# Optimization experiments

Hardware: AMD Instinct MI355X
Metric: run time of the kernel (lower is better)

The kernel has to match this reference:

```python
import jax, jax.numpy as jnp
import numpy as np

G = 4
EPS = 1e-5

def group_norm(x, gamma, beta):
    B, C, D, H, W = x.shape
    xg = x.reshape(B, G, C // G, D, H, W)
    mu = xg.mean(axis=(2, 3, 4, 5), keepdims=True)
    var = xg.var(axis=(2, 3, 4, 5), keepdims=True)
    xn = ((xg - mu) * jax.lax.rsqrt(var + EPS)).reshape(B, C, D, H, W)
    return xn * gamma[None, :, None, None, None] + beta[None, :, None, None, None]

def conv3d(x, w, b):
    y = jax.lax.conv_general_dilated(x, w, (1, 1, 1), [(1, 1), (1, 1), (1, 1)],
                                     dimension_numbers=('NCDHW', 'OIDHW', 'NCDHW'))
    return y + b[None, :, None, None, None]

def deform_conv_hw(x, offset, w, b):
    # x: [B,C,D,H,W]; offset: [B, 2*27, D,H,W] -> per-tap (dh, dw); depth taps are rigid.
    B, C, D, H, W = x.shape
    off = offset.reshape(B, 27, 2, D, H, W)
    xp = jnp.pad(x, ((0, 0), (0, 0), (1, 1), (0, 0), (0, 0)))  # zero-pad depth only
    hh = jnp.arange(H, dtype=x.dtype)[None, None, :, None]
    ww = jnp.arange(W, dtype=x.dtype)[None, None, None, :]
    bi = jnp.arange(B)[:, None, None, None]
    di = jnp.arange(D)[None, :, None, None]
    out = jnp.zeros((B, w.shape[0], D, H, W), x.dtype)
    tap = 0
    for i in range(3):
        x_d = xp[:, :, i:i + D]  # depth-shifted view [B,C,D,H,W]
        for j in range(3):
            for k in range(3):
                hp = hh + (j - 1) + off[:, tap, 0]  # [B,D,H,W] fractional h position
                wp = ww + (k - 1) + off[:, tap, 1]
                h0 = jnp.floor(hp); w0 = jnp.floor(wp)
                h0i = h0.astype(jnp.int32); w0i = w0.astype(jnp.int32)
                lh = hp - h0; lw = wp - w0
                def gather(hi, wi):
                    m = ((hi >= 0) & (hi < H) & (wi >= 0) & (wi < W)).astype(x.dtype)
                    g = x_d[bi, :, di, jnp.clip(hi, 0, H - 1), jnp.clip(wi, 0, W - 1)]  # [B,D,H,W,C]
                    return g, m
                g00, m00 = gather(h0i, w0i)
                g01, m01 = gather(h0i, w0i + 1)
                g10, m10 = gather(h0i + 1, w0i)
                g11, m11 = gather(h0i + 1, w0i + 1)
                val = (((1 - lh) * (1 - lw) * m00)[..., None] * g00
                       + ((1 - lh) * lw * m01)[..., None] * g01
                       + (lh * (1 - lw) * m10)[..., None] * g10
                       + (lh * lw * m11)[..., None] * g11)
                out = out + jnp.einsum('bdhwc,oc->bodhw', val, w[:, :, i, j, k])
                tap += 1
    return out + b[None, :, None, None, None]

def setup_inputs():
    key = jax.random.key(0)
    ks = jax.random.split(key, 8)
    B, C, D, H, W = 1, 32, 24, 96, 96
    x = jax.random.normal(ks[0], (B, C, D, H, W), jnp.float32)
    g1 = jnp.ones((C,), jnp.float32); be1 = jnp.zeros((C,), jnp.float32)
    g2 = jnp.ones((C,), jnp.float32); be2 = jnp.zeros((C,), jnp.float32)
    ow1 = jax.random.normal(ks[1], (54, C, 3, 3, 3), jnp.float32) * 0.02
    ob1 = jnp.zeros((54,), jnp.float32)
    dw1 = jax.random.normal(ks[2], (C, C, 3, 3, 3), jnp.float32) * 0.05
    db1 = jnp.zeros((C,), jnp.float32)
    ow2 = jax.random.normal(ks[3], (54, C, 3, 3, 3), jnp.float32) * 0.02
    ob2 = jnp.zeros((54,), jnp.float32)
    dw2 = jax.random.normal(ks[4], (C, C, 3, 3, 3), jnp.float32) * 0.05
    db2 = jnp.zeros((C,), jnp.float32)
    return {"x": x, "g1": g1, "be1": be1, "g2": g2, "be2": be2,
            "ow1": ow1, "ob1": ob1, "dw1": dw1, "db1": db1,
            "ow2": ow2, "ob2": ob2, "dw2": dw2, "db2": db2}

def reference(x, g1, be1, g2, be2, ow1, ob1, dw1, db1, ow2, ob2, dw2, db2):
    h = jax.nn.relu(group_norm(x, g1, be1))
    h = deform_conv_hw(h, conv3d(h, ow1, ob1), dw1, db1)
    h = jax.nn.relu(group_norm(h, g2, be2))
    h = deform_conv_hw(h, conv3d(h, ow2, ob2), dw2, db2)
    return h + x
```

## Files before the change

### kernel.cpp

```cpp
#include <hip/hip_runtime.h>
#include <hip/hip_fp16.h>

#define CC   32
#define DD   24
#define HH   96
#define WW   96
#define HWC  (HH*WW)
#define DHW  (DD*HH*WW)
#define NG   4
#define CPG  (CC/NG)
#define OC1  54
#define GN_EPS 1e-5f
#define NBLK2 (DHW/128)
#define CHUNK2 (NBLK2/8)

typedef float  f32x4 __attribute__((ext_vector_type(4)));
typedef _Float16 f16x8 __attribute__((ext_vector_type(8)));
typedef unsigned int u32x4 __attribute__((ext_vector_type(4)));

union F16Frag { f16x8 v; __half2 h2[4]; };

__device__ __forceinline__ int swz_block(int bid) {
    return (bid % 8) * CHUNK2 + (bid / 8);
}

__global__ void pack_w(const float* __restrict__ src, _Float16* __restrict__ dst,
                       int O, int NT, int n) {
    int idx = blockIdx.x * 256 + threadIdx.x;
    if (idx >= n) return;
    int e    = idx & 7;
    int lane = (idx >> 3) & 63;
    int nt   = (idx >> 9) % NT;
    int tap  = (idx >> 9) / NT;
    int o = nt * 16 + (lane & 15);
    int c = (lane >> 4) * 8 + e;
    float v = (o < O) ? src[(o * CC + c) * 27 + tap] : 0.f;
    dst[idx] = (_Float16)v;
}

__global__ void gn_stats(const float* __restrict__ x, float* __restrict__ stats) {
    const int g = blockIdx.x >> 5;
    const int s = blockIdx.x & 31;
    const float4* base = (const float4*)(x + (size_t)g * CPG * DHW);
    const int n4 = CPG * DHW / 4;
    float s1 = 0.f, s2 = 0.f;
    for (int idx = s * 256 + threadIdx.x; idx < n4; idx += 32 * 256) {
        float4 v = base[idx];
        s1 += v.x + v.y + v.z + v.w;
        s2 += v.x * v.x + v.y * v.y + v.z * v.z + v.w * v.w;
    }
    for (int off = 32; off > 0; off >>= 1) {
        s1 += __shfl_down(s1, off);
        s2 += __shfl_down(s2, off);
    }
    __shared__ float ls1[4], ls2[4];
    int wid = threadIdx.x >> 6;
    if ((threadIdx.x & 63) == 0) { ls1[wid] = s1; ls2[wid] = s2; }
    __syncthreads();
    if (threadIdx.x == 0) {
        float a = 0.f, b = 0.f;
        for (int i = 0; i < 4; i++) { a += ls1[i]; b += ls2[i]; }
        atomicAdd(&stats[g * 2 + 0], a);
        atomicAdd(&stats[g * 2 + 1], b);
    }
}

__global__ void gn_apply_T(const float* __restrict__ x, const float* __restrict__ stats,
                           const float* __restrict__ gamma, const float* __restrict__ beta,
                           __half* __restrict__ yT) {
    const int p = blockIdx.x * 256 + threadIdx.x;
    const float invN = 1.0f / (float)(CPG * DHW);
    float mean[NG], rstd[NG];
#pragma unroll
    for (int g = 0; g < NG; g++) {
        mean[g] = stats[2 * g] * invN;
        float var = stats[2 * g + 1] * invN - mean[g] * mean[g];
        rstd[g] = rsqrtf(var + GN_EPS);
    }
    float vals[CC];
#pragma unroll
    for (int c = 0; c < CC; c++) {
        const int g = c >> 3;
        const float ga = gamma[c] * rstd[g];
        const float be = beta[c] - mean[g] * ga;
        vals[c] = fmaxf(0.f, x[(size_t)c * DHW + p] * ga + be);
    }
    union { __half2 h2[16]; u32x4 q[4]; } u;
#pragma unroll
    for (int c = 0; c < 16; c++) u.h2[c] = __floats2half2_rn(vals[2 * c], vals[2 * c + 1]);
    u32x4* dst = (u32x4*)(yT + (size_t)p * CC);
#pragma unroll
    for (int q = 0; q < 4; q++) __builtin_nontemporal_store(u.q[q], dst + q);
}

__global__ __launch_bounds__(128) void offs_mfma(const __half* __restrict__ xT,
                                                 const _Float16* __restrict__ wB,
                                                 const float* __restrict__ bias,
                                                 __half* __restrict__ offF) {
    const int tid  = threadIdx.x;
    const int lane = tid & 63;
    const int wave = tid >> 6;
    const int p0   = swz_block(blockIdx.x) * 128;
    const int pw   = p0 + wave * 64;
    const int d    = pw / HWC;
    const int rem  = pw % HWC;
    const int mrow = lane & 15;
    const int kg   = lane >> 4;

    int hq[4], wq[4];
#pragma unroll
    for (int m = 0; m < 4; m++) {
        int rr = rem + m * 16 + mrow;
        hq[m] = rr / WW; wq[m] = rr % WW;
    }

    f32x4 acc[4][4];
#pragma unroll
    for (int m = 0; m < 4; m++)
#pragma unroll
        for (int n = 0; n < 4; n++) acc[m][n] = (f32x4){0.f, 0.f, 0.f, 0.f};

    const f16x8* wb8 = (const f16x8*)wB;

#pragma unroll 1
    for (int i = 0; i < 3; i++) {
        const int dd = d + i - 1;
        if ((unsigned)dd >= DD) continue;
        const __half* xd = xT + (size_t)dd * HWC * CC;
#pragma unroll 1
        for (int jk = 0; jk < 9; jk++) {
            const int j = jk / 3, k = jk % 3, tap = i * 9 + jk;
            const f16x8 b0 = wb8[(tap * 4 + 0) * 64 + lane];
            const f16x8 b1 = wb8[(tap * 4 + 1) * 64 + lane];
            const f16x8 b2 = wb8[(tap * 4 + 2) * 64 + lane];
            const f16x8 b3 = wb8[(tap * 4 + 3) * 64 + lane];
#pragma unroll
            for (int m = 0; m < 4; m++) {
                const int hh = hq[m] + j - 1;
                const int ww = wq[m] + k - 1;
                f16x8 a = {0, 0, 0, 0, 0, 0, 0, 0};
                if ((unsigned)hh < HH && (unsigned)ww < WW)
                    a = *(const f16x8*)(xd + (size_t)(hh * WW + ww) * CC + kg * 8);
                acc[m][0] = __builtin_amdgcn_mfma_f32_16x16x32_f16(a, b0, acc[m][0], 0, 0, 0);
                acc[m][1] = __builtin_amdgcn_mfma_f32_16x16x32_f16(a, b1, acc[m][1], 0, 0, 0);
                acc[m][2] = __builtin_amdgcn_mfma_f32_16x16x32_f16(a, b2, acc[m][2], 0, 0, 0);
                acc[m][3] = __builtin_amdgcn_mfma_f32_16x16x32_f16(a, b3, acc[m][3], 0, 0, 0);
            }
        }
    }

    __shared__ __align__(16) float lds[OC1 * 132];
#pragma unroll
    for (int m = 0; m < 4; m++)
#pragma unroll
        for (int nt = 0; nt < 4; nt++) {
            int o = nt * 16 + mrow;
            if (o < OC1)
                *(f32x4*)&lds[o * 132 + wave * 64 + m * 16 + kg * 4] = acc[m][nt];
        }
    __syncthreads();
#pragma unroll 1
    for (int o = 0; o < OC1; o++) {
        float v = lds[o * 132 + tid] + bias[o];
        offF[(size_t)o * DHW + p0 + tid] = __float2half(v);
    }
}

__global__ __launch_bounds__(128) void deform_mfma(const __half* __restrict__ xT,
                                                   const __half* __restrict__ offF,
                                                   const _Float16* __restrict__ wB,
                                                   const float* __restrict__ bias,
                                                   const float* __restrict__ resid,
                                                   float* __restrict__ outp) {
    const int tid  = threadIdx.x;
    const int lane = tid & 63;
    const int wave = tid >> 6;
    const int p0   = swz_block(blockIdx.x) * 128;
    const int pw   = p0 + wave * 64;
    const int d    = pw / HWC;
    const int rem  = pw % HWC;
    const int mrow = lane & 15;
    const int kg   = lane >> 4;

    int hq[4], wq[4];
#pragma unroll
    for (int m = 0; m < 4; m++) {
        int rr = rem + m * 16 + mrow;
        hq[m] = rr / WW; wq[m] = rr % WW;
    }

    f32x4 acc[4][2];
#pragma unroll
    for (int m = 0; m < 4; m++) {
        acc[m][0] = (f32x4){0.f, 0.f, 0.f, 0.f};
        acc[m][1] = (f32x4){0.f, 0.f, 0.f, 0.f};
    }

    const f16x8* wb8 = (const f16x8*)wB;

#pragma unroll 1
    for (int i = 0; i < 3; i++) {
        const int dd = d + i - 1;
        if ((unsigned)dd >= DD) continue;
        const __half* xd = xT + (size_t)dd * HWC * CC;
#pragma unroll 1
        for (int jk = 0; jk < 9; jk++) {
            const int j = jk / 3, k = jk % 3, tap = i * 9 + jk;
            const f16x8 b0 = wb8[(tap * 2 + 0) * 64 + lane];
            const f16x8 b1 = wb8[(tap * 2 + 1) * 64 + lane];
            const __half* offh = offF + (size_t)(tap * 2 + 0) * DHW;
            const __half* offw = offF + (size_t)(tap * 2 + 1) * DHW;
#pragma unroll
            for (int m = 0; m < 4; m++) {
                const int pq = pw + m * 16 + mrow;
                const float oh = __half2float(offh[pq]);
                const float ov = __half2float(offw[pq]);
                const float hp  = (float)(hq[m] + j - 1) + oh;
                const float wpf = (float)(wq[m] + k - 1) + ov;
                const float h0f = floorf(hp), w0f = floorf(wpf);
                const int h0 = (int)h0f, w0 = (int)w0f;
                const float lh = hp - h0f, lw = wpf - w0f;
                const bool hv0 = (h0 >= 0) && (h0 < HH);
                const bool hv1 = (h0 >= -1) && (h0 < HH - 1);
                const bool wv0 = (w0 >= 0) && (w0 < WW);
                const bool wv1 = (w0 >= -1) && (w0 < WW - 1);
                const float c00 = (hv0 && wv0) ? (1.f - lh) * (1.f - lw) : 0.f;
                const float c01 = (hv0 && wv1) ? (1.f - lh) * lw : 0.f;
                const float c10 = (hv1 && wv0) ? lh * (1.f - lw) : 0.f;
                const float c11 = (hv1 && wv1) ? lh * lw : 0.f;
                const int h0c = min(max(h0, 0), HH - 1);
                const int h1c = min(max(h0 + 1, 0), HH - 1);
                const int w0c = min(max(w0, 0), WW - 1);
                const int w1c = min(max(w0 + 1, 0), WW - 1);
                F16Frag a00, a01, a10, a11, A;
                a00.v = *(const f16x8*)(xd + (size_t)(h0c * WW + w0c) * CC + kg * 8);
                a01.v = *(const f16x8*)(xd + (size_t)(h0c * WW + w1c) * CC + kg * 8);
                a10.v = *(const f16x8*)(xd + (size_t)(h1c * WW + w0c) * CC + kg * 8);
                a11.v = *(const f16x8*)(xd + (size_t)(h1c * WW + w1c) * CC + kg * 8);
                const __half2 C00 = __float2half2_rn(c00);
                const __half2 C01 = __float2half2_rn(c01);
                const __half2 C10 = __float2half2_rn(c10);
                const __half2 C11 = __float2half2_rn(c11);
#pragma unroll
                for (int r = 0; r < 4; r++) {
                    __half2 t = __hmul2(C00, a00.h2[r]);
                    t = __hfma2(C01, a01.h2[r], t);
                    t = __hfma2(C10, a10.h2[r], t);
                    t = __hfma2(C11, a11.h2[r], t);
                    A.h2[r] = t;
                }
                acc[m][0] = __builtin_amdgcn_mfma_f32_16x16x32_f16(A.v, b0, acc[m][0], 0, 0, 0);
                acc[m][1] = __builtin_amdgcn_mfma_f32_16x16x32_f16(A.v, b1, acc[m][1], 0, 0, 0);
            }
        }
    }

    __shared__ __align__(16) float lds[CC * 132];
#pragma unroll
    for (int m = 0; m < 4; m++)
#pragma unroll
        for (int nt = 0; nt < 2; nt++) {
            int o = nt * 16 + mrow;
            *(f32x4*)&lds[o * 132 + wave * 64 + m * 16 + kg * 4] = acc[m][nt];
        }
    __syncthreads();
    if (resid) {
#pragma unroll 1
        for (int o = 0; o < CC; o++) {
            float v = lds[o * 132 + tid] + bias[o] + resid[(size_t)o * DHW + p0 + tid];
            outp[(size_t)o * DHW + p0 + tid] = v;
        }
    } else {
#pragma unroll 1
        for (int o = 0; o < CC; o++) {
            float v = lds[o * 132 + tid] + bias[o];
            outp[(size_t)o * DHW + p0 + tid] = v;
        }
    }
}

extern "C" void kernel_launch(void* const* d_in, const int* in_sizes, int n_in,
                              void* d_out, int out_size, void* d_ws, size_t ws_size,
                              hipStream_t stream) {
    const float* x   = (const float*)d_in[0];
    const float* g1  = (const float*)d_in[1];
    const float* be1 = (const float*)d_in[2];
    const float* g2  = (const float*)d_in[3];
    const float* be2 = (const float*)d_in[4];
    const float* ow1 = (const float*)d_in[5];
    const float* ob1 = (const float*)d_in[6];
    const float* dw1 = (const float*)d_in[7];
    const float* db1 = (const float*)d_in[8];
    const float* ow2 = (const float*)d_in[9];
    const float* ob2 = (const float*)d_in[10];
    const float* dw2 = (const float*)d_in[11];
    const float* db2 = (const float*)d_in[12];
    float* out = (float*)d_out;
    float* ws  = (float*)d_ws;

    float*    stats = ws;
    _Float16* wBo1  = (_Float16*)(ws + 256);
    _Float16* wBd1  = (_Float16*)(ws + 27904);
    _Float16* wBo2  = (_Float16*)(ws + 41728);
    _Float16* wBd2  = (_Float16*)(ws + 69376);
    __half*   hT    = (__half*)(ws + 83200);
    __half*   offF  = (__half*)(ws + 3622144);

    (void)hipMemsetAsync(stats, 0, 16 * sizeof(float), stream);
    pack_w<<<(27 * 4 * 512 + 255) / 256, 256, 0, stream>>>(ow1, wBo1, 54, 4, 27 * 4 * 512);
    pack_w<<<(27 * 2 * 512 + 255) / 256, 256, 0, stream>>>(dw1, wBd1, 32, 2, 27 * 2 * 512);
    pack_w<<<(27 * 4 * 512 + 255) / 256, 256, 0, stream>>>(ow2, wBo2, 54, 4, 27 * 4 * 512);
    pack_w<<<(27 * 2 * 512 + 255) / 256, 256, 0, stream>>>(dw2, wBd2, 32, 2, 27 * 2 * 512);

    gn_stats<<<NG * 32, 256, 0, stream>>>(x, stats + 0);
    gn_apply_T<<<DHW / 256, 256, 0, stream>>>(x, stats + 0, g1, be1, hT);
    offs_mfma<<<NBLK2, 128, 0, stream>>>(hT, wBo1, ob1, offF);
    deform_mfma<<<NBLK2, 128, 0, stream>>>(hT, offF, wBd1, db1, nullptr, out);

    gn_stats<<<NG * 32, 256, 0, stream>>>(out, stats + 8);
    gn_apply_T<<<DHW / 256, 256, 0, stream>>>(out, stats + 8, g2, be2, hT);
    offs_mfma<<<NBLK2, 128, 0, stream>>>(hT, wBo2, ob2, offF);
    deform_mfma<<<NBLK2, 128, 0, stream>>>(hT, offF, wBd2, db2, x, out);
}
```

Measured before the change: 426.7 us.

## Fuse offset conv and deformable conv into one kernel with LDS-resident offsets

Merges the offset-predicting conv and the deformable conv into a single kernel. Each wave keeps its 54 fp16 offset channels in LDS rather than writing them to global memory and reading them back. It also swizzles gn_apply block order, switches its stores from nontemporal to regular so the transposed tensor stays cached for the conv, and batches the gather loads ahead of the MFMAs. The cost is higher register pressure, since both accumulator sets are live under launch_bounds(128,3), plus an extra barrier per block.

```diff
diff --git a/kernel.cpp b/kernel.cpp
--- a/kernel.cpp
+++ b/kernel.cpp
@@ -11,8 +11,11 @@
 #define CPG  (CC/NG)
 #define OC1  54
 #define GN_EPS 1e-5f
-#define NBLK2 (DHW/128)
-#define CHUNK2 (NBLK2/8)
+
+#define NBLK_F (DHW/128)
+#define CHUNK_F (NBLK_F/8)
+#define NBLK_G (DHW/256)
+#define CHUNK_G (NBLK_G/8)
 
 typedef float  f32x4 __attribute__((ext_vector_type(4)));
 typedef _Float16 f16x8 __attribute__((ext_vector_type(8)));
@@ -20,8 +23,8 @@
 
 union F16Frag { f16x8 v; __half2 h2[4]; };
 
-__device__ __forceinline__ int swz_block(int bid) {
-    return (bid % 8) * CHUNK2 + (bid / 8);
+__device__ __forceinline__ int swz(int bid, int chunk) {
+    return (bid % 8) * chunk + (bid / 8);
 }
 
 __global__ void pack_w(const float* __restrict__ src, _Float16* __restrict__ dst,
@@ -68,7 +71,7 @@
 __global__ void gn_apply_T(const float* __restrict__ x, const float* __restrict__ stats,
                            const float* __restrict__ gamma, const float* __restrict__ beta,
                            __half* __restrict__ yT) {
-    const int p = blockIdx.x * 256 + threadIdx.x;
+    const int p = swz(blockIdx.x, CHUNK_G) * 256 + threadIdx.x;
     const float invN = 1.0f / (float)(CPG * DHW);
     float mean[NG], rstd[NG];
 #pragma unroll
@@ -90,22 +93,31 @@
     for (int c = 0; c < 16; c++) u.h2[c] = __floats2half2_rn(vals[2 * c], vals[2 * c + 1]);
     u32x4* dst = (u32x4*)(yT + (size_t)p * CC);
 #pragma unroll
-    for (int q = 0; q < 4; q++) __builtin_nontemporal_store(u.q[q], dst + q);
-}
-
-__global__ __launch_bounds__(128) void offs_mfma(const __half* __restrict__ xT,
-                                                 const _Float16* __restrict__ wB,
-                                                 const float* __restrict__ bias,
-                                                 __half* __restrict__ offF) {
+    for (int q = 0; q < 4; q++) dst[q] = u.q[q];
+}
+
+#define OPAD 70
+__global__ __launch_bounds__(128, 3) void fused_conv(const __half* __restrict__ xT,
+                                                     const _Float16* __restrict__ wBo,
+                                                     const float* __restrict__ ob,
+                                                     const _Float16* __restrict__ wBd,
+                                                     const float* __restrict__ db,
+                                                     const float* __restrict__ resid,
+                                                     float* __restrict__ outp) {
+    __shared__ __align__(16) char lds_raw[CC * 132 * 4];
+    __half* offs_lds = (__half*)lds_raw;
+    float*  out_lds  = (float*)lds_raw;
+
     const int tid  = threadIdx.x;
     const int lane = tid & 63;
     const int wave = tid >> 6;
-    const int p0   = swz_block(blockIdx.x) * 128;
+    const int p0   = swz(blockIdx.x, CHUNK_F) * 128;
     const int pw   = p0 + wave * 64;
     const int d    = pw / HWC;
     const int rem  = pw % HWC;
     const int mrow = lane & 15;
     const int kg   = lane >> 4;
+    const int wbase = wave * (OC1 * OPAD);
 
     int hq[4], wq[4];
 #pragma unroll
@@ -114,89 +126,75 @@
         hq[m] = rr / WW; wq[m] = rr % WW;
     }
 
-    f32x4 acc[4][4];
+    f32x4 aco[4][4];
 #pragma unroll
     for (int m = 0; m < 4; m++)
 #pragma unroll
-        for (int n = 0; n < 4; n++) acc[m][n] = (f32x4){0.f, 0.f, 0.f, 0.f};
-
-    const f16x8* wb8 = (const f16x8*)wB;
+        for (int n = 0; n < 4; n++) aco[m][n] = (f32x4){0.f, 0.f, 0.f, 0.f};
+
+    const f16x8* wbo8 = (const f16x8*)wBo;
 
 #pragma unroll 1
     for (int i = 0; i < 3; i++) {
         const int dd = d + i - 1;
         if ((unsigned)dd >= DD) continue;
         const __half* xd = xT + (size_t)dd * HWC * CC;
-#pragma unroll 1
+#pragma unroll 3
         for (int jk = 0; jk < 9; jk++) {
             const int j = jk / 3, k = jk % 3, tap = i * 9 + jk;
-            const f16x8 b0 = wb8[(tap * 4 + 0) * 64 + lane];
-            const f16x8 b1 = wb8[(tap * 4 + 1) * 64 + lane];
-            const f16x8 b2 = wb8[(tap * 4 + 2) * 64 + lane];
-            const f16x8 b3 = wb8[(tap * 4 + 3) * 64 + lane];
+            const f16x8 b0 = wbo8[(tap * 4 + 0) * 64 + lane];
+            const f16x8 b1 = wbo8[(tap * 4 + 1) * 64 + lane];
+            const f16x8 b2 = wbo8[(tap * 4 + 2) * 64 + lane];
+            const f16x8 b3 = wbo8[(tap * 4 + 3) * 64 + lane];
+            f16x8 a[4];
 #pragma unroll
             for (int m = 0; m < 4; m++) {
                 const int hh = hq[m] + j - 1;
                 const int ww = wq[m] + k - 1;
-                f16x8 a = {0, 0, 0, 0, 0, 0, 0, 0};
+                a[m] = (f16x8){0, 0, 0, 0, 0, 0, 0, 0};
                 if ((unsigned)hh < HH && (unsigned)ww < WW)
-                    a = *(const f16x8*)(xd + (size_t)(hh * WW + ww) * CC + kg * 8);
-                acc[m][0] = __builtin_amdgcn_mfma_f32_16x16x32_f16(a, b0, acc[m][0], 0, 0, 0);
-                acc[m][1] = __builtin_amdgcn_mfma_f32_16x16x32_f16(a, b1, acc[m][1], 0, 0, 0);
-                acc[m][2] = __builtin_amdgcn_mfma_f32_16x16x32_f16(a, b2, acc[m][2], 0, 0, 0);
-                acc[m][3] = __builtin_amdgcn_mfma_f32_16x16x32_f16(a, b3, acc[m][3], 0, 0, 0);
-            }
-        }
-    }
-
-    __shared__ __align__(16) float lds[OC1 * 132];
-#pragma unroll
-    for (int m = 0; m < 4; m++)
+                    a[m] = *(const f16x8*)(xd + (size_t)(hh * WW + ww) * CC + kg * 8);
+            }
+#pragma unroll
+            for (int m = 0; m < 4; m++) {
+                aco[m][0] = __builtin_amdgcn_mfma_f32_16x16x32_f16(a[m], b0, aco[m][0], 0, 0, 0);
+                aco[m][1] = __builtin_amdgcn_mfma_f32_16x16x32_f16(a[m], b1, aco[m][1], 0, 0, 0);
+                aco[m][2] = __builtin_amdgcn_mfma_f32_16x16x32_f16(a[m], b2, aco[m][2], 0, 0, 0);
+                aco[m][3] = __builtin_amdgcn_mfma_f32_16x16x32_f16(a[m], b3, aco[m][3], 0, 0, 0);
+            }
+        }
+    }
+
+    float bo[4];
+#pragma unroll
+    for (int nt = 0; nt < 4; nt++) {
+        const int o = nt * 16 + mrow;
+        bo[nt] = (o < OC1) ? ob[o] : 0.f;
+    }
+#pragma unroll
+    for (int m = 0; m < 4; m++) {
 #pragma unroll
         for (int nt = 0; nt < 4; nt++) {
-            int o = nt * 16 + mrow;
-            if (o < OC1)
-                *(f32x4*)&lds[o * 132 + wave * 64 + m * 16 + kg * 4] = acc[m][nt];
-        }
+            const int o = nt * 16 + mrow;
+            if (o < OC1) {
+                const int idx = wbase + o * OPAD + m * 16 + kg * 4;
+                __half2 lo = __floats2half2_rn(aco[m][nt].x + bo[nt], aco[m][nt].y + bo[nt]);
+                __half2 hi = __floats2half2_rn(aco[m][nt].z + bo[nt], aco[m][nt].w + bo[nt]);
+                *(__half2*)&offs_lds[idx]     = lo;
+                *(__half2*)&offs_lds[idx + 2] = hi;
+            }
+        }
+    }
     __syncthreads();
-#pragma unroll 1
-    for (int o = 0; o < OC1; o++) {
-        float v = lds[o * 132 + tid] + bias[o];
-        offF[(size_t)o * DHW + p0 + tid] = __float2half(v);
-    }
-}
-
-__global__ __launch_bounds__(128) void deform_mfma(const __half* __restrict__ xT,
-                                                   const __half* __restrict__ offF,
-                                                   const _Float16* __restrict__ wB,
-                                                   const float* __restrict__ bias,
-                                                   const float* __restrict__ resid,
-                                                   float* __restrict__ outp) {
-    const int tid  = threadIdx.x;
-    const int lane = tid & 63;
-    const int wave = tid >> 6;
-    const int p0   = swz_block(blockIdx.x) * 128;
-    const int pw   = p0 + wave * 64;
-    const int d    = pw / HWC;
-    const int rem  = pw % HWC;
-    const int mrow = lane & 15;
-    const int kg   = lane >> 4;
-
-    int hq[4], wq[4];
+
+    f32x4 acd[4][2];
 #pragma unroll
     for (int m = 0; m < 4; m++) {
-        int rr = rem + m * 16 + mrow;
-        hq[m] = rr / WW; wq[m] = rr % WW;
-    }
-
-    f32x4 acc[4][2];
-#pragma unroll
-    for (int m = 0; m < 4; m++) {
-        acc[m][0] = (f32x4){0.f, 0.f, 0.f, 0.f};
-        acc[m][1] = (f32x4){0.f, 0.f, 0.f, 0.f};
-    }
-
-    const f16x8* wb8 = (const f16x8*)wB;
+        acd[m][0] = (f32x4){0.f, 0.f, 0.f, 0.f};
+        acd[m][1] = (f32x4){0.f, 0.f, 0.f, 0.f};
+    }
+
+    const f16x8* wbd8 = (const f16x8*)wBd;
 
 #pragma unroll 1
     for (int i = 0; i < 3; i++) {
@@ -206,15 +204,15 @@
 #pragma unroll 1
         for (int jk = 0; jk < 9; jk++) {
             const int j = jk / 3, k = jk % 3, tap = i * 9 + jk;
-            const f16x8 b0 = wb8[(tap * 2 + 0) * 64 + lane];
-            const f16x8 b1 = wb8[(tap * 2 + 1) * 64 + lane];
-            const __half* offh = offF + (size_t)(tap * 2 + 0) * DHW;
-            const __half* offw = offF + (size_t)(tap * 2 + 1) * DHW;
+            const f16x8 b0 = wbd8[(tap * 2 + 0) * 64 + lane];
+            const f16x8 b1 = wbd8[(tap * 2 + 1) * 64 + lane];
+            int i00[4], i01[4], i10[4], i11[4];
+            float c00[4], c01[4], c10[4], c11[4];
 #pragma unroll
             for (int m = 0; m < 4; m++) {
-                const int pq = pw + m * 16 + mrow;
-                const float oh = __half2float(offh[pq]);
-                const float ov = __half2float(offw[pq]);
+                const int ptl = m * 16 + mrow;
+                const float oh = __half2float(offs_lds[wbase + (2 * tap + 0) * OPAD + ptl]);
+                const float ov = __half2float(offs_lds[wbase + (2 * tap + 1) * OPAD + ptl]);
                 const float hp  = (float)(hq[m] + j - 1) + oh;
                 const float wpf = (float)(wq[m] + k - 1) + ov;
                 const float h0f = floorf(hp), w0f = floorf(wpf);
@@ -224,23 +222,30 @@
                 const bool hv1 = (h0 >= -1) && (h0 < HH - 1);
                 const bool wv0 = (w0 >= 0) && (w0 < WW);
                 const bool wv1 = (w0 >= -1) && (w0 < WW - 1);
-                const float c00 = (hv0 && wv0) ? (1.f - lh) * (1.f - lw) : 0.f;
-                const float c01 = (hv0 && wv1) ? (1.f - lh) * lw : 0.f;
-                const float c10 = (hv1 && wv0) ? lh * (1.f - lw) : 0.f;
-                const float c11 = (hv1 && wv1) ? lh * lw : 0.f;
+                c00[m] = (hv0 && wv0) ? (1.f - lh) * (1.f - lw) : 0.f;
+                c01[m] = (hv0 && wv1) ? (1.f - lh) * lw : 0.f;
+                c10[m] = (hv1 && wv0) ? lh * (1.f - lw) : 0.f;
+                c11[m] = (hv1 && wv1) ? lh * lw : 0.f;
                 const int h0c = min(max(h0, 0), HH - 1);
                 const int h1c = min(max(h0 + 1, 0), HH - 1);
                 const int w0c = min(max(w0, 0), WW - 1);
                 const int w1c = min(max(w0 + 1, 0), WW - 1);
+                i00[m] = h0c * WW + w0c;
+                i01[m] = h0c * WW + w1c;
+                i10[m] = h1c * WW + w0c;
+                i11[m] = h1c * WW + w1c;
+            }
+#pragma unroll
+            for (int m = 0; m < 4; m++) {
                 F16Frag a00, a01, a10, a11, A;
-                a00.v = *(const f16x8*)(xd + (size_t)(h0c * WW + w0c) * CC + kg * 8);
-                a01.v = *(const f16x8*)(xd + (size_t)(h0c * WW + w1c) * CC + kg * 8);
-                a10.v = *(const f16x8*)(xd + (size_t)(h1c * WW + w0c) * CC + kg * 8);
-                a11.v = *(const f16x8*)(xd + (size_t)(h1c * WW + w1c) * CC + kg * 8);
-                const __half2 C00 = __float2half2_rn(c00);
-                const __half2 C01 = __float2half2_rn(c01);
-                const __half2 C10 = __float2half2_rn(c10);
-                const __half2 C11 = __float2half2_rn(c11);
+                a00.v = *(const f16x8*)(xd + (size_t)i00[m] * CC + kg * 8);
+                a01.v = *(const f16x8*)(xd + (size_t)i01[m] * CC + kg * 8);
+                a10.v = *(const f16x8*)(xd + (size_t)i10[m] * CC + kg * 8);
+                a11.v = *(const f16x8*)(xd + (size_t)i11[m] * CC + kg * 8);
+                const __half2 C00 = __float2half2_rn(c00[m]);
+                const __half2 C01 = __float2half2_rn(c01[m]);
+                const __half2 C10 = __float2half2_rn(c10[m]);
+                const __half2 C11 = __float2half2_rn(c11[m]);
 #pragma unroll
                 for (int r = 0; r < 4; r++) {
                     __half2 t = __hmul2(C00, a00.h2[r]);
@@ -249,33 +254,31 @@
                     t = __hfma2(C11, a11.h2[r], t);
                     A.h2[r] = t;
                 }
-                acc[m][0] = __builtin_amdgcn_mfma_f32_16x16x32_f16(A.v, b0, acc[m][0], 0, 0, 0);
-                acc[m][1] = __builtin_amdgcn_mfma_f32_16x16x32_f16(A.v, b1, acc[m][1], 0, 0, 0);
-            }
-        }
-    }
-
-    __shared__ __align__(16) float lds[CC * 132];
+                acd[m][0] = __builtin_amdgcn_mfma_f32_16x16x32_f16(A.v, b0, acd[m][0], 0, 0, 0);
+                acd[m][1] = __builtin_amdgcn_mfma_f32_16x16x32_f16(A.v, b1, acd[m][1], 0, 0, 0);
+            }
+        }
+    }
+    __syncthreads();
+
 #pragma unroll
     for (int m = 0; m < 4; m++)
 #pragma unroll
         for (int nt = 0; nt < 2; nt++) {
-            int o = nt * 16 + mrow;
-            *(f32x4*)&lds[o * 132 + wave * 64 + m * 16 + kg * 4] = acc[m][nt];
+            const int o = nt * 16 + mrow;
+            *(f32x4*)&out_lds[o * 132 + wave * 64 + m * 16 + kg * 4] = acd[m][nt];
         }
     __syncthreads();
     if (resid) {
 #pragma unroll 1
         for (int o = 0; o < CC; o++) {
-            float v = lds[o * 132 + tid] + bias[o] + resid[(size_t)o * DHW + p0 + tid];
+            float v = out_lds[o * 132 + tid] + db[o] + resid[(size_t)o * DHW + p0 + tid];
             outp[(size_t)o * DHW + p0 + tid] = v;
         }
     } else {
 #pragma unroll 1
-        for (int o = 0; o < CC; o++) {
-            float v = lds[o * 132 + tid] + bias[o];
-            outp[(size_t)o * DHW + p0 + tid] = v;
-        }
+        for (int o = 0; o < CC; o++)
+            outp[(size_t)o * DHW + p0 + tid] = out_lds[o * 132 + tid] + db[o];
     }
 }
 
@@ -304,7 +307,6 @@
     _Float16* wBo2  = (_Float16*)(ws + 41728);
     _Float16* wBd2  = (_Float16*)(ws + 69376);
     __half*   hT    = (__half*)(ws + 83200);
-    __half*   offF  = (__half*)(ws + 3622144);
 
     (void)hipMemsetAsync(stats, 0, 16 * sizeof(float), stream);
     pack_w<<<(27 * 4 * 512 + 255) / 256, 256, 0, stream>>>(ow1, wBo1, 54, 4, 27 * 4 * 512);
@@ -313,12 +315,10 @@
     pack_w<<<(27 * 2 * 512 + 255) / 256, 256, 0, stream>>>(dw2, wBd2, 32, 2, 27 * 2 * 512);
 
     gn_stats<<<NG * 32, 256, 0, stream>>>(x, stats + 0);
-    gn_apply_T<<<DHW / 256, 256, 0, stream>>>(x, stats + 0, g1, be1, hT);
-    offs_mfma<<<NBLK2, 128, 0, stream>>>(hT, wBo1, ob1, offF);
-    deform_mfma<<<NBLK2, 128, 0, stream>>>(hT, offF, wBd1, db1, nullptr, out);
+    gn_apply_T<<<NBLK_G, 256, 0, stream>>>(x, stats + 0, g1, be1, hT);
+    fused_conv<<<NBLK_F, 128, 0, stream>>>(hT, wBo1, ob1, wBd1, db1, nullptr, out);
 
     gn_stats<<<NG * 32, 256, 0, stream>>>(out, stats + 8);
-    gn_apply_T<<<DHW / 256, 256, 0, stream>>>(out, stats + 8, g2, be2, hT);
-    offs_mfma<<<NBLK2, 128, 0, stream>>>(hT, wBo2, ob2, offF);
-    deform_mfma<<<NBLK2, 128, 0, stream>>>(hT, offF, wBd2, db2, x, out);
-}
+    gn_apply_T<<<NBLK_G, 256, 0, stream>>>(out, stats + 8, g2, be2, hT);
+    fused_conv<<<NBLK_F, 128, 0, stream>>>(hT, wBo2, ob2, wBd2, db2, x, out);
+}
```

Result: faster. 367.4 us (-13.9%).
